# Kernel tuning notes

Measured on AMD Instinct MI355X. Metric: run time of the kernel, lower is better.

## Reference

```python
import jax, jax.numpy as jnp
import numpy as np

N_NODES = 100000
N_EDGES = 1600000
F_IN, F_HID, F_OUT = 512, 128, 64


def add_self_loops(edge_index, num_nodes):
    loop = jnp.arange(num_nodes, dtype=edge_index.dtype)
    loops = jnp.stack([loop, loop])  # [2, N]
    return jnp.concatenate([edge_index, loops], axis=1)


def gcn_conv(x, edge_index_sl, W, b, num_nodes):
    # x: [N, F_in], edge_index_sl: [2, E+N] (self-loops included)
    h = x @ W  # [N, F_out] transform before propagation (PyG GCNConv order)
    src, dst = edge_index_sl[0], edge_index_sl[1]
    ones = jnp.ones(src.shape[0], dtype=h.dtype)
    deg = jax.ops.segment_sum(ones, dst, num_segments=num_nodes)  # in-degree w/ self-loops
    dinv = jnp.where(deg > 0, jax.lax.rsqrt(deg), 0.0)
    norm = dinv[src] * dinv[dst]  # [E+N] symmetric normalization
    msg = h[src] * norm[:, None]  # gather + scale
    out = jax.ops.segment_sum(msg, dst, num_segments=num_nodes)  # scatter-add
    return out + b


def setup_inputs() -> dict:
    key = jax.random.key(0)
    k = jax.random.split(key, 6)
    x = jax.random.normal(k[0], (N_NODES, F_IN), dtype=jnp.float32)
    edge_index = jax.random.randint(k[1], (2, N_EDGES), 0, N_NODES, dtype=jnp.int64)
    W1 = jax.random.normal(k[2], (F_IN, F_HID), dtype=jnp.float32) * (1.0 / np.sqrt(F_IN))
    b1 = jnp.zeros((F_HID,), dtype=jnp.float32)
    W2 = jax.random.normal(k[3], (F_HID, F_OUT), dtype=jnp.float32) * (1.0 / np.sqrt(F_HID))
    b2 = jnp.zeros((F_OUT,), dtype=jnp.float32)
    return {"x": x, "edge_index": edge_index, "W1": W1, "b1": b1, "W2": W2, "b2": b2}


def reference(x, edge_index, W1, b1, W2, b2):
    ei = add_self_loops(edge_index, N_NODES)
    h = jax.nn.relu(gcn_conv(x, ei, W1, b1, N_NODES))
    out = gcn_conv(h, ei, W2, b2, N_NODES)
    return out
```

## Files before the change

### kernel.cpp

```cpp
#include <hip/hip_runtime.h>

#define N_NODES 100000
#define N_EDGES 1600000
#define F_IN 512
#define F_HID 128
#define F_OUT 64

#define BSH 8
#define NBUK 391

typedef unsigned int u32;
typedef __attribute__((ext_vector_type(8))) short bf16x8;
typedef __attribute__((ext_vector_type(4))) float f32x4;

__device__ float g7_bf2f(unsigned short u) {
    return __uint_as_float(((unsigned int)u) << 16);
}

__device__ unsigned short g7_f2bf(float f) {
    unsigned int u = __float_as_uint(f);
    u = u + 0x7fffu + ((u >> 16) & 1u);
    return (unsigned short)(u >> 16);
}

__device__ float2 g7_up(unsigned int u) {
    float2 r;
    r.x = __uint_as_float(u << 16);
    r.y = __uint_as_float(u & 0xffff0000u);
    return r;
}

__device__ static inline void g7_gl2lds16(const void* g, void* l) {
    __builtin_amdgcn_global_load_lds(
        (const __attribute__((address_space(1))) u32*)g,
        (__attribute__((address_space(3))) u32*)l, 16, 0, 0);
}

__global__ void GCN_16716012716713_kernel() {}

__global__ void g7_zero(int* p, int n) {
    int i = blockIdx.x * blockDim.x + threadIdx.x;
    if (i < n) p[i] = 0;
}

__global__ void g7_iprobe(const int* raw, int* iflag) {
    __shared__ int s[256];
    int tid = threadIdx.x;
    int f = 0;
    for (int i = tid; i < 1024; i += 256) {
        if (raw[2 * i + 1] != 0) f = 1;
    }
    s[tid] = f;
    __syncthreads();
    for (int off = 128; off > 0; off >>= 1) {
        if (tid < off) s[tid] |= s[tid + off];
        __syncthreads();
    }
    if (tid == 0) iflag[0] = s[0];
}

__global__ void g7_fprobe(const unsigned int* xw, int* fflag) {
    __shared__ int s[256];
    int tid = threadIdx.x;
    int cnt = 0;
    for (int i = tid; i < 4096; i += 256) {
        unsigned int lo = xw[i] & 0xffffu;
        unsigned int e = (lo >> 7) & 0xffu;
        if (e >= 110u && e <= 140u) cnt = cnt + 1;
    }
    s[tid] = cnt;
    __syncthreads();
    for (int off = 128; off > 0; off >>= 1) {
        if (tid < off) s[tid] += s[tid + off];
        __syncthreads();
    }
    if (tid == 0) fflag[0] = (s[0] > 2048) ? 1 : 0;
}

__global__ void g7_pack(const int* raw, const int* iflag, int* ei, int* deg) {
    int i = blockIdx.x * blockDim.x + threadIdx.x;
    if (i < 2 * N_EDGES) {
        int v;
        if (iflag[0] == 0) {
            v = raw[2 * i];
        } else {
            v = raw[i];
        }
        ei[i] = v;
        if (i >= N_EDGES) atomicAdd(&deg[v], 1);
    }
}

__global__ void g7_cvt(const void* src, const int* fflag, float* dst, int n) {
    int i = blockIdx.x * blockDim.x + threadIdx.x;
    if (i < n) {
        if (fflag[0] == 1) {
            dst[i] = g7_bf2f(((const unsigned short*)src)[i]);
        } else {
            dst[i] = ((const float*)src)[i];
        }
    }
}

__global__ void g7_w1s(const void* W1, const int* fflag,
                       unsigned short* W1Th, unsigned short* W1Tl) {
    int i = blockIdx.x * blockDim.x + threadIdx.x;
    if (i < F_IN * F_HID) {
        int k = i >> 7;
        int n = i & 127;
        float w;
        if (fflag[0] == 1) {
            w = g7_bf2f(((const unsigned short*)W1)[i]);
        } else {
            w = ((const float*)W1)[i];
        }
        unsigned short hi = g7_f2bf(w);
        unsigned short lo = g7_f2bf(w - g7_bf2f(hi));
        W1Th[n * F_IN + k] = hi;
        W1Tl[n * F_IN + k] = lo;
    }
}

__global__ void g7_dinv(const int* deg, float* dinv) {
    int i = blockIdx.x * blockDim.x + threadIdx.x;
    if (i < N_NODES) {
        dinv[i] = rsqrtf((float)deg[i] + 1.0f);
    }
}

__global__ void g7_bsum(const int* deg, int* bsum) {
    __shared__ int s[256];
    int i = blockIdx.x * 256 + threadIdx.x;
    s[threadIdx.x] = (i < N_NODES) ? deg[i] : 0;
    __syncthreads();
    for (int off = 128; off > 0; off >>= 1) {
        if (threadIdx.x < off) s[threadIdx.x] += s[threadIdx.x + off];
        __syncthreads();
    }
    if (threadIdx.x == 0) bsum[blockIdx.x] = s[0];
}

__global__ void g7_bscan(const int* bsum, int* boff, int nblk, int* rowptr) {
    __shared__ int s[512];
    int tid = threadIdx.x;
    int v = (tid < nblk) ? bsum[tid] : 0;
    s[tid] = v;
    __syncthreads();
    for (int off = 1; off < 512; off <<= 1) {
        int t = (tid >= off) ? s[tid - off] : 0;
        __syncthreads();
        s[tid] += t;
        __syncthreads();
    }
    if (tid < nblk) boff[tid] = s[tid] - v;
    if (tid == nblk - 1) rowptr[N_NODES] = s[tid];
}

__global__ void g7_scan(const int* deg, const int* boff, int* rowptr) {
    __shared__ int s[256];
    int i = blockIdx.x * 256 + threadIdx.x;
    int v = (i < N_NODES) ? deg[i] : 0;
    s[threadIdx.x] = v;
    __syncthreads();
    for (int off = 1; off < 256; off <<= 1) {
        int t = (threadIdx.x >= off) ? s[threadIdx.x - off] : 0;
        __syncthreads();
        s[threadIdx.x] += t;
        __syncthreads();
    }
    if (i < N_NODES) {
        rowptr[i] = s[threadIdx.x] - v + boff[blockIdx.x];
    }
}

__global__ void g7_binit(const int* rowptr, int* bcur) {
    int b = blockIdx.x * blockDim.x + threadIdx.x;
    if (b < NBUK) bcur[b] = rowptr[b << BSH];
}

#define P1_EPT 32
#define P1_TILE (256 * P1_EPT)
__global__ void g7_part1(const int* ei, int* bcur, uint2* part) {
    __shared__ int cnt[NBUK + 1];
    __shared__ int base[NBUK + 1];
    int tid = threadIdx.x;
    long long t0 = (long long)blockIdx.x * P1_TILE;
    for (int i = tid; i < NBUK; i += 256) cnt[i] = 0;
    __syncthreads();
#pragma unroll 4
    for (int r = 0; r < P1_EPT; ++r) {
        long long e = t0 + r * 256 + tid;
        if (e < N_EDGES) {
            int d = ei[N_EDGES + e];
            atomicAdd(&cnt[d >> BSH], 1);
        }
    }
    __syncthreads();
    for (int i = tid; i < NBUK; i += 256) {
        int c = cnt[i];
        base[i] = (c > 0) ? atomicAdd(&bcur[i], c) : 0;
        cnt[i] = 0;
    }
    __syncthreads();
#pragma unroll 4
    for (int r = 0; r < P1_EPT; ++r) {
        long long e = t0 + r * 256 + tid;
        if (e < N_EDGES) {
            int s = ei[e];
            int d = ei[N_EDGES + e];
            int bk = d >> BSH;
            int off = atomicAdd(&cnt[bk], 1);
            uint2 p; p.x = (u32)s; p.y = (u32)d;
            part[(long long)base[bk] + off] = p;
        }
    }
}

__global__ void g7_part2(const int* rowptr, const uint2* part, int* csr) {
    __shared__ int lcur[256];
    int b = blockIdx.x;
    int tid = threadIdx.x;
    int n0 = b << BSH;
    int n1 = n0 + 256; if (n1 > N_NODES) n1 = N_NODES;
    if (tid < 256) {
        int node = n0 + tid;
        lcur[tid] = (node < N_NODES) ? rowptr[node] : 0;
    }
    __syncthreads();
    int beg = rowptr[n0];
    int end = rowptr[n1];
    for (int j = beg + tid; j < end; j += 512) {
        uint2 p = part[j];
        int pos = atomicAdd(&lcur[p.y - n0], 1);
        csr[pos] = (int)p.x;
    }
}

__global__ __launch_bounds__(256, 2) void g7_gemm1s(const void* x, const int* fflag,
        const unsigned short* W1Th, const unsigned short* W1Tl, unsigned short* h1b) {
    __shared__ uint4 smv[4096];
    char* smc = (char*)smv;
    int tid = threadIdx.x;
    int m0 = blockIdx.x * 128;
    int w = tid >> 6;
    int lane = tid & 63;
    int wr = w >> 1, wc = w & 1;
    int la = lane & 15;
    int lk = lane >> 4;
    int isbf = fflag[0];
    int ar = tid >> 1;
    int ah = tid & 1;

    f32x4 acc[4][4];
#pragma unroll
    for (int i = 0; i < 4; ++i)
#pragma unroll
        for (int j = 0; j < 4; ++j) acc[i][j] = (f32x4){0.f, 0.f, 0.f, 0.f};

    uint4 rA[4];

    auto loadA = [&](int k0) {
        int m = m0 + ar;
        if (m >= N_NODES) m = N_NODES - 1;
        if (isbf) {
            const char* s = (const char*)x + ((long long)m * F_IN + k0 + ah * 16) * 2;
            rA[0] = *(const uint4*)s;
            rA[1] = *(const uint4*)(s + 16);
        } else {
            const char* s = (const char*)x + ((long long)m * F_IN + k0 + ah * 16) * 4;
            rA[0] = *(const uint4*)s;
            rA[1] = *(const uint4*)(s + 16);
            rA[2] = *(const uint4*)(s + 32);
            rA[3] = *(const uint4*)(s + 48);
        }
    };

    auto writeA = [&](char* As) {
        float f[16];
        if (isbf) {
            const unsigned short* p = (const unsigned short*)rA;
#pragma unroll
            for (int j = 0; j < 16; ++j) f[j] = g7_bf2f(p[j]);
        } else {
            const float* p = (const float*)rA;
#pragma unroll
            for (int j = 0; j < 16; ++j) f[j] = p[j];
        }
        unsigned int hw[8], lw[8];
#pragma unroll
        for (int j = 0; j < 8; ++j) {
            unsigned short h0 = g7_f2bf(f[2 * j]);
            unsigned short h1v = g7_f2bf(f[2 * j + 1]);
            unsigned short l0 = g7_f2bf(f[2 * j] - g7_bf2f(h0));
            unsigned short l1 = g7_f2bf(f[2 * j + 1] - g7_bf2f(h1v));
            hw[j] = (unsigned int)h0 | ((unsigned int)h1v << 16);
            lw[j] = (unsigned int)l0 | ((unsigned int)l1 << 16);
        }
        int swz = (ar & 7) << 4;
        char* dst = As + ar * 128;
        *(uint4*)(dst + ((ah * 32 + 0) ^ swz))      = make_uint4(hw[0], hw[1], hw[2], hw[3]);
        *(uint4*)(dst + ((ah * 32 + 16) ^ swz))     = make_uint4(hw[4], hw[5], hw[6], hw[7]);
        *(uint4*)(dst + ((64 + ah * 32 + 0) ^ swz)) = make_uint4(lw[0], lw[1], lw[2], lw[3]);
        *(uint4*)(dst + ((64 + ah * 32 + 16) ^ swz))= make_uint4(lw[4], lw[5], lw[6], lw[7]);
    };

    auto stageB = [&](char* Bs, int k0) {
#pragma unroll
        for (int p = 0; p < 4; ++p) {
            int nr = w * 32 + p * 8 + (lane >> 3);
            int cp = ((lane & 7) * 16) ^ (((lane >> 3) & 7) << 4);
            const char* src = (cp < 64)
                ? (const char*)W1Th + (long long)nr * 1024 + k0 * 2 + cp
                : (const char*)W1Tl + (long long)nr * 1024 + k0 * 2 + (cp - 64);
            g7_gl2lds16(src, Bs + (w * 32 + p * 8) * 128);
        }
    };

    auto compute = [&](const char* As, const char* Bs) {
        bf16x8 a_hi[4], a_lo[4], b_hi[4], b_lo[4];
#pragma unroll
        for (int i = 0; i < 4; ++i) {
            int r = wr * 64 + i * 16 + la;
            int swz = (r & 7) << 4;
            const char* ab = As + r * 128;
            a_hi[i] = *(const bf16x8*)(ab + ((lk * 16) ^ swz));
            a_lo[i] = *(const bf16x8*)(ab + ((64 + lk * 16) ^ swz));
            int n = wc * 64 + i * 16 + la;
            int swzb = (n & 7) << 4;
            const char* bb = Bs + n * 128;
            b_hi[i] = *(const bf16x8*)(bb + ((lk * 16) ^ swzb));
            b_lo[i] = *(const bf16x8*)(bb + ((64 + lk * 16) ^ swzb));
        }
#pragma unroll
        for (int i = 0; i < 4; ++i)
#pragma unroll
            for (int j = 0; j < 4; ++j) {
                acc[i][j] = __builtin_amdgcn_mfma_f32_16x16x32_bf16(
                    a_hi[i], b_hi[j], acc[i][j], 0, 0, 0);
                acc[i][j] = __builtin_amdgcn_mfma_f32_16x16x32_bf16(
                    a_lo[i], b_hi[j], acc[i][j], 0, 0, 0);
                acc[i][j] = __builtin_amdgcn_mfma_f32_16x16x32_bf16(
                    a_hi[i], b_lo[j], acc[i][j], 0, 0, 0);
            }
    };

    loadA(0);
    stageB(smc + 16384, 0);
    writeA(smc);
    __syncthreads();

    for (int kt = 0; kt < 16; ++kt) {
        char* bc = smc + (kt & 1) * 32768;
        char* bn = smc + ((kt & 1) ^ 1) * 32768;
        if (kt < 15) {
            loadA((kt + 1) * 32);
            stageB(bn + 16384, (kt + 1) * 32);
        }
        compute(bc, bc + 16384);
        if (kt < 15) writeA(bn);
        __syncthreads();
    }

#pragma unroll
    for (int i = 0; i < 4; ++i) {
#pragma unroll
        for (int j = 0; j < 4; ++j) {
            int n = wc * 64 + j * 16 + la;
#pragma unroll
            for (int q = 0; q < 4; ++q) {
                int m = m0 + wr * 64 + i * 16 + lk * 4 + q;
                if (m < N_NODES) {
                    h1b[(long long)m * F_HID + n] = g7_f2bf(acc[i][j][q]);
                }
            }
        }
    }
}

__global__ void g7_agg1(const int* rowptr, const int* csr, const float* dinv,
                        const unsigned short* h1b, const float* b1, float* r1) {
    int node = blockIdx.x * 4 + (threadIdx.x >> 6);
    int lane = threadIdx.x & 63;
    int e = lane >> 5;
    int fl = lane & 31;
    if (node >= N_NODES) return;
    int beg = rowptr[node];
    int end = rowptr[node + 1];
    const uint2* hv = (const uint2*)h1b;
    float a0 = 0.f, a1 = 0.f, a2 = 0.f, a3 = 0.f;
    int j = beg + e;
    for (; j + 2 < end; j += 4) {
        int s0 = csr[j];
        int s1 = csr[j + 2];
        float w0 = dinv[s0];
        float w1 = dinv[s1];
        uint2 v0 = hv[(long long)s0 * 32 + fl];
        uint2 v1 = hv[(long long)s1 * 32 + fl];
        float2 p0 = g7_up(v0.x), q0 = g7_up(v0.y);
        float2 p1 = g7_up(v1.x), q1 = g7_up(v1.y);
        a0 += p0.x * w0 + p1.x * w1;
        a1 += p0.y * w0 + p1.y * w1;
        a2 += q0.x * w0 + q1.x * w1;
        a3 += q0.y * w0 + q1.y * w1;
    }
    if (j < end) {
        int s0 = csr[j];
        float w0 = dinv[s0];
        uint2 v0 = hv[(long long)s0 * 32 + fl];
        float2 p0 = g7_up(v0.x), q0 = g7_up(v0.y);
        a0 += p0.x * w0;
        a1 += p0.y * w0;
        a2 += q0.x * w0;
        a3 += q0.y * w0;
    }
    float di = dinv[node];
    if (e == 0) {
        uint2 vd = hv[(long long)node * 32 + fl];
        float2 pd = g7_up(vd.x), qd = g7_up(vd.y);
        a0 += pd.x * di;
        a1 += pd.y * di;
        a2 += qd.x * di;
        a3 += qd.y * di;
    }
    a0 += __shfl_xor(a0, 32);
    a1 += __shfl_xor(a1, 32);
    a2 += __shfl_xor(a2, 32);
    a3 += __shfl_xor(a3, 32);
    if (e == 0) {
        float4 bb = *(const float4*)(b1 + 4 * fl);
        float r0 = a0 * di + bb.x;
        float r1v = a1 * di + bb.y;
        float r2 = a2 * di + bb.z;
        float r3 = a3 * di + bb.w;
        if (r0 < 0.f) r0 = 0.f;
        if (r1v < 0.f) r1v = 0.f;
        if (r2 < 0.f) r2 = 0.f;
        if (r3 < 0.f) r3 = 0.f;
        float4 o;
        o.x = r0; o.y = r1v; o.z = r2; o.w = r3;
        *(float4*)(r1 + (long long)node * F_HID + 4 * fl) = o;
    }
}

__global__ void g7_gemm2(const float* r1, const float* W2, unsigned short* h2b) {
    __shared__ float Rs[32][68];
    __shared__ float Ws[32][64];
    int tid = threadIdx.x;
    int m0 = blockIdx.x * 64;
    int tx = tid & 15;
    int ty = tid >> 4;
    float acc[4][4];
#pragma unroll
    for (int i = 0; i < 4; ++i) {
#pragma unroll
        for (int j = 0; j < 4; ++j) acc[i][j] = 0.0f;
    }

    for (int k0 = 0; k0 < F_HID; k0 += 32) {
#pragma unroll
        for (int r = 0; r < 8; ++r) {
            int i = r * 256 + tid;
            int kk = i & 31;
            int mm = i >> 5;
            int m = m0 + mm;
            float v = 0.0f;
            if (m < N_NODES) {
                v = r1[(long long)m * F_HID + k0 + kk];
            }
            Rs[kk][mm] = v;
        }
#pragma unroll
        for (int r = 0; r < 8; ++r) {
            int i = r * 256 + tid;
            int wk = i >> 6;
            int wn = i & 63;
            Ws[wk][wn] = W2[(k0 + wk) * F_OUT + wn];
        }
        __syncthreads();
#pragma unroll
        for (int k = 0; k < 32; ++k) {
            float a[4];
            float b[4];
#pragma unroll
            for (int i = 0; i < 4; ++i) a[i] = Rs[k][ty * 4 + i];
#pragma unroll
            for (int j = 0; j < 4; ++j) b[j] = Ws[k][tx * 4 + j];
#pragma unroll
            for (int i = 0; i < 4; ++i) {
#pragma unroll
                for (int j = 0; j < 4; ++j) acc[i][j] += a[i] * b[j];
            }
        }
        __syncthreads();
    }
#pragma unroll
    for (int i = 0; i < 4; ++i) {
        int m = m0 + ty * 4 + i;
        if (m < N_NODES) {
            unsigned int w0 = (unsigned int)g7_f2bf(acc[i][0])
                            | ((unsigned int)g7_f2bf(acc[i][1]) << 16);
            unsigned int w1 = (unsigned int)g7_f2bf(acc[i][2])
                            | ((unsigned int)g7_f2bf(acc[i][3]) << 16);
            uint2 o; o.x = w0; o.y = w1;
            *(uint2*)(h2b + (long long)m * F_OUT + tx * 4) = o;
        }
    }
}

__global__ void g7_agg2(const int* rowptr, const int* csr, const float* dinv,
                        const unsigned short* h2b, const float* b2, const int* fflag,
                        void* out) {
    int node = blockIdx.x * 4 + (threadIdx.x >> 6);
    int lane = threadIdx.x & 63;
    int e = lane >> 5;
    int fl = lane & 31;
    if (node >= N_NODES) return;
    int beg = rowptr[node];
    int end = rowptr[node + 1];
    const u32* hv = (const u32*)h2b;
    float a0 = 0.f, a1 = 0.f;
    int j = beg + e;
    for (; j + 2 < end; j += 4) {
        int s0 = csr[j];
        int s1 = csr[j + 2];
        float w0 = dinv[s0];
        float w1 = dinv[s1];
        u32 v0 = hv[(long long)s0 * 32 + fl];
        u32 v1 = hv[(long long)s1 * 32 + fl];
        float2 p0 = g7_up(v0);
        float2 p1 = g7_up(v1);
        a0 += p0.x * w0 + p1.x * w1;
        a1 += p0.y * w0 + p1.y * w1;
    }
    if (j < end) {
        int s0 = csr[j];
        float w0 = dinv[s0];
        u32 v0 = hv[(long long)s0 * 32 + fl];
        float2 p0 = g7_up(v0);
        a0 += p0.x * w0;
        a1 += p0.y * w0;
    }
    float di = dinv[node];
    if (e == 0) {
        u32 vd = hv[(long long)node * 32 + fl];
        float2 pd = g7_up(vd);
        a0 += pd.x * di;
        a1 += pd.y * di;
    }
    a0 += __shfl_xor(a0, 32);
    a1 += __shfl_xor(a1, 32);
    if (e == 0) {
        float v0 = a0 * di + b2[2 * fl];
        float v1 = a1 * di + b2[2 * fl + 1];
        long long oi = (long long)node * F_OUT + 2 * fl;
        if (fflag[0] == 1) {
            u32 o = (u32)g7_f2bf(v0) | ((u32)g7_f2bf(v1) << 16);
            *(u32*)((unsigned short*)out + oi) = o;
        } else {
            float2 o; o.x = v0; o.y = v1;
            *(float2*)((float*)out + oi) = o;
        }
    }
}

extern "C" void kernel_launch(void* const* d_in, const int* in_sizes, int n_in,
                              void* d_out, int out_size, void* d_ws, size_t ws_size,
                              hipStream_t stream) {
    const void* x     = d_in[0];
    const int* ei_raw = (const int*)d_in[1];
    const void* W1    = d_in[2];
    const void* b1    = d_in[3];
    const void* W2    = d_in[4];
    const void* b2    = d_in[5];

    const int NBLK = (N_NODES + 255) / 256;

    char* ws = (char*)d_ws;
    int*   deg    = (int*)(ws + 0);
    int*   iflag  = (int*)(ws + 409600);
    int*   fflag  = (int*)(ws + 409616);
    int*   bsum   = (int*)(ws + 409632);
    int*   boff   = (int*)(ws + 412800);
    int*   bcur   = (int*)(ws + 450560);
    float* dinv   = (float*)(ws + 524288);
    unsigned short* W1Th = (unsigned short*)(ws + 1048576);
    unsigned short* W1Tl = (unsigned short*)(ws + 1179648);
    float* b1f    = (float*)(ws + 1310720);
    float* W2f    = (float*)(ws + 1311232);
    float* b2f    = (float*)(ws + 1344000);
    int*   ei     = (int*)(ws + 2097152);
    int*   rowptr = (int*)(ws + 14897152);
    int*   csr    = (int*)(ws + 16777216);
    unsigned short* h1b = (unsigned short*)(ws + 23177216);
    uint2* part   = (uint2*)(ws + 50331648);
    float* r1     = (float*)(ws + 74377216);
    unsigned short* h2b = (unsigned short*)(ws + 125577216);

    g7_zero<<<(N_NODES + 255) / 256, 256, 0, stream>>>(deg, N_NODES);

    g7_iprobe<<<1, 256, 0, stream>>>(ei_raw, iflag);
    g7_fprobe<<<1, 256, 0, stream>>>((const unsigned int*)x, fflag);

    g7_pack<<<(2 * N_EDGES + 255) / 256, 256, 0, stream>>>(ei_raw, iflag, ei, deg);

    g7_cvt<<<1, 128, 0, stream>>>(b1, fflag, b1f, F_HID);
    g7_cvt<<<(F_HID * F_OUT + 255) / 256, 256, 0, stream>>>(W2, fflag, W2f, F_HID * F_OUT);
    g7_cvt<<<1, 64, 0, stream>>>(b2, fflag, b2f, F_OUT);
    g7_w1s<<<(F_IN * F_HID + 255) / 256, 256, 0, stream>>>(W1, fflag, W1Th, W1Tl);

    g7_dinv<<<(N_NODES + 255) / 256, 256, 0, stream>>>(deg, dinv);

    g7_bsum<<<NBLK, 256, 0, stream>>>(deg, bsum);
    g7_bscan<<<1, 512, 0, stream>>>(bsum, boff, NBLK, rowptr);
    g7_scan<<<NBLK, 256, 0, stream>>>(deg, boff, rowptr);

    g7_binit<<<(NBUK + 255) / 256, 256, 0, stream>>>(rowptr, bcur);
    g7_part1<<<(N_EDGES + P1_TILE - 1) / P1_TILE, 256, 0, stream>>>(ei, bcur, part);
    g7_part2<<<NBUK, 512, 0, stream>>>(rowptr, part, csr);

    g7_gemm1s<<<(N_NODES + 127) / 128, 256, 0, stream>>>(x, fflag, W1Th, W1Tl, h1b);

    g7_agg1<<<N_NODES / 4, 256, 0, stream>>>(rowptr, csr, dinv, h1b, b1f, r1);

    g7_gemm2<<<(N_NODES + 63) / 64, 256, 0, stream>>>(r1, W2f, h2b);

    g7_agg2<<<N_NODES / 4, 256, 0, stream>>>(rowptr, csr, dinv, h2b, b2f, fflag, d_out);
}
```

Measured before the change: 648.5 us.

## Single-buffer LDS in gemm1 and raise occupancy to four blocks per CU

The first GEMM kernel goes from a double-buffered 64KB LDS layout to a single 32KB A/B buffer. Prefetching now happens through two register buffers for A, and launch bounds rise from 2 to 4 blocks per CU. The goal is to hide memory latency through higher occupancy instead of LDS double buffering. In exchange, each k-step now needs two barriers, the B global-to-LDS copy is no longer overlapped with compute, and the tighter register budget may cause spills.

```diff
diff --git a/kernel.cpp b/kernel.cpp
--- a/kernel.cpp
+++ b/kernel.cpp
@@ -236,10 +236,11 @@
     }
 }
 
-__global__ __launch_bounds__(256, 2) void g7_gemm1s(const void* x, const int* fflag,
+__global__ __launch_bounds__(256, 4) void g7_gemm1s(const void* x, const int* fflag,
         const unsigned short* W1Th, const unsigned short* W1Tl, unsigned short* h1b) {
-    __shared__ uint4 smv[4096];
-    char* smc = (char*)smv;
+    __shared__ uint4 smv[2048];
+    char* As = (char*)smv;
+    char* Bs = As + 16384;
     int tid = threadIdx.x;
     int m0 = blockIdx.x * 128;
     int w = tid >> 6;
@@ -257,9 +258,9 @@
 #pragma unroll
         for (int j = 0; j < 4; ++j) acc[i][j] = (f32x4){0.f, 0.f, 0.f, 0.f};
 
-    uint4 rA[4];
-
-    auto loadA = [&](int k0) {
+    uint4 rA0[4], rA1[4];
+
+    auto loadA = [&](uint4* rA, int k0) {
         int m = m0 + ar;
         if (m >= N_NODES) m = N_NODES - 1;
         if (isbf) {
@@ -275,7 +276,7 @@
         }
     };
 
-    auto writeA = [&](char* As) {
+    auto writeA = [&](const uint4* rA) {
         float f[16];
         if (isbf) {
             const unsigned short* p = (const unsigned short*)rA;
@@ -304,7 +305,7 @@
         *(uint4*)(dst + ((64 + ah * 32 + 16) ^ swz))= make_uint4(lw[4], lw[5], lw[6], lw[7]);
     };
 
-    auto stageB = [&](char* Bs, int k0) {
+    auto stageB = [&](int k0) {
 #pragma unroll
         for (int p = 0; p < 4; ++p) {
             int nr = w * 32 + p * 8 + (lane >> 3);
@@ -316,7 +317,7 @@
         }
     };
 
-    auto compute = [&](const char* As, const char* Bs) {
+    auto compute = [&]() {
         bf16x8 a_hi[4], a_lo[4], b_hi[4], b_lo[4];
 #pragma unroll
         for (int i = 0; i < 4; ++i) {
@@ -344,20 +345,20 @@
             }
     };
 
-    loadA(0);
-    stageB(smc + 16384, 0);
-    writeA(smc);
-    __syncthreads();
-
-    for (int kt = 0; kt < 16; ++kt) {
-        char* bc = smc + (kt & 1) * 32768;
-        char* bn = smc + ((kt & 1) ^ 1) * 32768;
-        if (kt < 15) {
-            loadA((kt + 1) * 32);
-            stageB(bn + 16384, (kt + 1) * 32);
-        }
-        compute(bc, bc + 16384);
-        if (kt < 15) writeA(bn);
+    loadA(rA0, 0);
+#pragma unroll
+    for (int kt = 0; kt < 16; kt += 2) {
+        writeA(rA0);
+        stageB(kt * 32);
+        __syncthreads();
+        loadA(rA1, (kt + 1) * 32);
+        compute();
+        __syncthreads();
+        writeA(rA1);
+        stageB((kt + 1) * 32);
+        __syncthreads();
+        if (kt + 2 < 16) loadA(rA0, (kt + 2) * 32);
+        compute();
         __syncthreads();
     }
 
```

Measured after the change: 732.7 us. 13.0% more time.

## Use 512-thread GEMM1 blocks with smaller per-wave tiles and fuse weight-prep kernels

Applied to the files above, without the earlier changes.

The first GEMM now runs 8 waves per 128x128 tile instead of 4, so each wave owns a 64x32 output sub-tile with half the accumulators. Each thread loads and splits half as much A data. The launch bound moves from (256,2) to (512,4) to raise occupancy and latency hiding. Separately, the three small conversion kernels and the W1 split kernel are merged into a single prep launch to cut launch overhead. With more waves per tile, A fragments are reloaded from shared memory by more waves, which adds LDS traffic.

```diff
diff --git a/kernel.cpp b/kernel.cpp
--- a/kernel.cpp
+++ b/kernel.cpp
@@ -91,25 +91,16 @@
     }
 }
 
-__global__ void g7_cvt(const void* src, const int* fflag, float* dst, int n) {
+__global__ void g7_prep(const void* W1, const void* W2, const void* b1, const void* b2,
+                        const int* fflag, unsigned short* W1Th, unsigned short* W1Tl,
+                        float* W2f, float* b1f, float* b2f) {
     int i = blockIdx.x * blockDim.x + threadIdx.x;
-    if (i < n) {
-        if (fflag[0] == 1) {
-            dst[i] = g7_bf2f(((const unsigned short*)src)[i]);
-        } else {
-            dst[i] = ((const float*)src)[i];
-        }
-    }
-}
-
-__global__ void g7_w1s(const void* W1, const int* fflag,
-                       unsigned short* W1Th, unsigned short* W1Tl) {
-    int i = blockIdx.x * blockDim.x + threadIdx.x;
+    int isbf = fflag[0];
     if (i < F_IN * F_HID) {
         int k = i >> 7;
         int n = i & 127;
         float w;
-        if (fflag[0] == 1) {
+        if (isbf == 1) {
             w = g7_bf2f(((const unsigned short*)W1)[i]);
         } else {
             w = ((const float*)W1)[i];
@@ -118,6 +109,18 @@
         unsigned short lo = g7_f2bf(w - g7_bf2f(hi));
         W1Th[n * F_IN + k] = hi;
         W1Tl[n * F_IN + k] = lo;
+    } else if (i < F_IN * F_HID + F_HID * F_OUT) {
+        int j = i - F_IN * F_HID;
+        W2f[j] = (isbf == 1) ? g7_bf2f(((const unsigned short*)W2)[j])
+                             : ((const float*)W2)[j];
+    } else if (i < F_IN * F_HID + F_HID * F_OUT + F_HID) {
+        int j = i - F_IN * F_HID - F_HID * F_OUT;
+        b1f[j] = (isbf == 1) ? g7_bf2f(((const unsigned short*)b1)[j])
+                             : ((const float*)b1)[j];
+    } else if (i < F_IN * F_HID + F_HID * F_OUT + F_HID + F_OUT) {
+        int j = i - F_IN * F_HID - F_HID * F_OUT - F_HID;
+        b2f[j] = (isbf == 1) ? g7_bf2f(((const unsigned short*)b2)[j])
+                             : ((const float*)b2)[j];
     }
 }
 
@@ -236,7 +239,7 @@
     }
 }
 
-__global__ __launch_bounds__(256, 2) void g7_gemm1s(const void* x, const int* fflag,
+__global__ __launch_bounds__(512, 4) void g7_gemm1s(const void* x, const int* fflag,
         const unsigned short* W1Th, const unsigned short* W1Tl, unsigned short* h1b) {
     __shared__ uint4 smv[4096];
     char* smc = (char*)smv;
@@ -244,51 +247,48 @@
     int m0 = blockIdx.x * 128;
     int w = tid >> 6;
     int lane = tid & 63;
-    int wr = w >> 1, wc = w & 1;
+    int wr = w >> 2, wc = w & 3;
     int la = lane & 15;
     int lk = lane >> 4;
     int isbf = fflag[0];
-    int ar = tid >> 1;
-    int ah = tid & 1;
-
-    f32x4 acc[4][4];
+    int ar = tid >> 2;
+    int ah = tid & 3;
+
+    f32x4 acc[4][2];
 #pragma unroll
     for (int i = 0; i < 4; ++i)
 #pragma unroll
-        for (int j = 0; j < 4; ++j) acc[i][j] = (f32x4){0.f, 0.f, 0.f, 0.f};
-
-    uint4 rA[4];
+        for (int j = 0; j < 2; ++j) acc[i][j] = (f32x4){0.f, 0.f, 0.f, 0.f};
+
+    uint4 rA[2];
 
     auto loadA = [&](int k0) {
         int m = m0 + ar;
         if (m >= N_NODES) m = N_NODES - 1;
         if (isbf) {
-            const char* s = (const char*)x + ((long long)m * F_IN + k0 + ah * 16) * 2;
+            const char* s = (const char*)x + ((long long)m * F_IN + k0 + ah * 8) * 2;
+            rA[0] = *(const uint4*)s;
+        } else {
+            const char* s = (const char*)x + ((long long)m * F_IN + k0 + ah * 8) * 4;
             rA[0] = *(const uint4*)s;
             rA[1] = *(const uint4*)(s + 16);
-        } else {
-            const char* s = (const char*)x + ((long long)m * F_IN + k0 + ah * 16) * 4;
-            rA[0] = *(const uint4*)s;
-            rA[1] = *(const uint4*)(s + 16);
-            rA[2] = *(const uint4*)(s + 32);
-            rA[3] = *(const uint4*)(s + 48);
         }
     };
 
     auto writeA = [&](char* As) {
-        float f[16];
+        float f[8];
         if (isbf) {
-            const unsigned short* p = (const unsigned short*)rA;
-#pragma unroll
-            for (int j = 0; j < 16; ++j) f[j] = g7_bf2f(p[j]);
+            const unsigned short* p = (const unsigned short*)&rA[0];
+#pragma unroll
+            for (int j = 0; j < 8; ++j) f[j] = g7_bf2f(p[j]);
         } else {
             const float* p = (const float*)rA;
 #pragma unroll
-            for (int j = 0; j < 16; ++j) f[j] = p[j];
-        }
-        unsigned int hw[8], lw[8];
-#pragma unroll
-        for (int j = 0; j < 8; ++j) {
+            for (int j = 0; j < 8; ++j) f[j] = p[j];
+        }
+        unsigned int hw[4], lw[4];
+#pragma unroll
+        for (int j = 0; j < 4; ++j) {
             unsigned short h0 = g7_f2bf(f[2 * j]);
             unsigned short h1v = g7_f2bf(f[2 * j + 1]);
             unsigned short l0 = g7_f2bf(f[2 * j] - g7_bf2f(h0));
@@ -298,50 +298,49 @@
         }
         int swz = (ar & 7) << 4;
         char* dst = As + ar * 128;
-        *(uint4*)(dst + ((ah * 32 + 0) ^ swz))      = make_uint4(hw[0], hw[1], hw[2], hw[3]);
-        *(uint4*)(dst + ((ah * 32 + 16) ^ swz))     = make_uint4(hw[4], hw[5], hw[6], hw[7]);
-        *(uint4*)(dst + ((64 + ah * 32 + 0) ^ swz)) = make_uint4(lw[0], lw[1], lw[2], lw[3]);
-        *(uint4*)(dst + ((64 + ah * 32 + 16) ^ swz))= make_uint4(lw[4], lw[5], lw[6], lw[7]);
+        *(uint4*)(dst + ((ah * 16) ^ swz))      = make_uint4(hw[0], hw[1], hw[2], hw[3]);
+        *(uint4*)(dst + ((64 + ah * 16) ^ swz)) = make_uint4(lw[0], lw[1], lw[2], lw[3]);
     };
 
     auto stageB = [&](char* Bs, int k0) {
 #pragma unroll
-        for (int p = 0; p < 4; ++p) {
-            int nr = w * 32 + p * 8 + (lane >> 3);
+        for (int p = 0; p < 2; ++p) {
+            int nr = w * 16 + p * 8 + (lane >> 3);
             int cp = ((lane & 7) * 16) ^ (((lane >> 3) & 7) << 4);
             const char* src = (cp < 64)
                 ? (const char*)W1Th + (long long)nr * 1024 + k0 * 2 + cp
                 : (const char*)W1Tl + (long long)nr * 1024 + k0 * 2 + (cp - 64);
-            g7_gl2lds16(src, Bs + (w * 32 + p * 8) * 128);
+            g7_gl2lds16(src, Bs + (w * 16 + p * 8) * 128);
         }
     };
 
     auto compute = [&](const char* As, const char* Bs) {
-        bf16x8 a_hi[4], a_lo[4], b_hi[4], b_lo[4];
+        bf16x8 bh[2], bl[2];
+#pragma unroll
+        for (int j = 0; j < 2; ++j) {
+            int n = wc * 32 + j * 16 + la;
+            int swzb = (n & 7) << 4;
+            const char* bb = Bs + n * 128;
+            bh[j] = *(const bf16x8*)(bb + ((lk * 16) ^ swzb));
+            bl[j] = *(const bf16x8*)(bb + ((64 + lk * 16) ^ swzb));
+        }
 #pragma unroll
         for (int i = 0; i < 4; ++i) {
             int r = wr * 64 + i * 16 + la;
             int swz = (r & 7) << 4;
             const char* ab = As + r * 128;
-            a_hi[i] = *(const bf16x8*)(ab + ((lk * 16) ^ swz));
-            a_lo[i] = *(const bf16x8*)(ab + ((64 + lk * 16) ^ swz));
-            int n = wc * 64 + i * 16 + la;
-            int swzb = (n & 7) << 4;
-            const char* bb = Bs + n * 128;
-            b_hi[i] = *(const bf16x8*)(bb + ((lk * 16) ^ swzb));
-            b_lo[i] = *(const bf16x8*)(bb + ((64 + lk * 16) ^ swzb));
-        }
-#pragma unroll
-        for (int i = 0; i < 4; ++i)
-#pragma unroll
-            for (int j = 0; j < 4; ++j) {
+            bf16x8 ah_ = *(const bf16x8*)(ab + ((lk * 16) ^ swz));
+            bf16x8 al_ = *(const bf16x8*)(ab + ((64 + lk * 16) ^ swz));
+#pragma unroll
+            for (int j = 0; j < 2; ++j) {
                 acc[i][j] = __builtin_amdgcn_mfma_f32_16x16x32_bf16(
-                    a_hi[i], b_hi[j], acc[i][j], 0, 0, 0);
+                    ah_, bh[j], acc[i][j], 0, 0, 0);
                 acc[i][j] = __builtin_amdgcn_mfma_f32_16x16x32_bf16(
-                    a_lo[i], b_hi[j], acc[i][j], 0, 0, 0);
+                    al_, bh[j], acc[i][j], 0, 0, 0);
                 acc[i][j] = __builtin_amdgcn_mfma_f32_16x16x32_bf16(
-                    a_hi[i], b_lo[j], acc[i][j], 0, 0, 0);
+                    ah_, bl[j], acc[i][j], 0, 0, 0);
             }
+        }
     };
 
     loadA(0);
@@ -364,8 +363,8 @@
 #pragma unroll
     for (int i = 0; i < 4; ++i) {
 #pragma unroll
-        for (int j = 0; j < 4; ++j) {
-            int n = wc * 64 + j * 16 + la;
+        for (int j = 0; j < 2; ++j) {
+            int n = wc * 32 + j * 16 + la;
 #pragma unroll
             for (int q = 0; q < 4; ++q) {
                 int m = m0 + wr * 64 + i * 16 + lk * 4 + q;
@@ -603,10 +602,9 @@
 
     g7_pack<<<(2 * N_EDGES + 255) / 256, 256, 0, stream>>>(ei_raw, iflag, ei, deg);
 
-    g7_cvt<<<1, 128, 0, stream>>>(b1, fflag, b1f, F_HID);
-    g7_cvt<<<(F_HID * F_OUT + 255) / 256, 256, 0, stream>>>(W2, fflag, W2f, F_HID * F_OUT);
-    g7_cvt<<<1, 64, 0, stream>>>(b2, fflag, b2f, F_OUT);
-    g7_w1s<<<(F_IN * F_HID + 255) / 256, 256, 0, stream>>>(W1, fflag, W1Th, W1Tl);
+    const int PREP_N = F_IN * F_HID + F_HID * F_OUT + F_HID + F_OUT;
+    g7_prep<<<(PREP_N + 255) / 256, 256, 0, stream>>>(W1, W2, b1, b2, fflag,
+                                                      W1Th, W1Tl, W2f, b1f, b2f);
 
     g7_dinv<<<(N_NODES + 255) / 256, 256, 0, stream>>>(deg, dinv);
 
@@ -618,7 +616,7 @@
     g7_part1<<<(N_EDGES + P1_TILE - 1) / P1_TILE, 256, 0, stream>>>(ei, bcur, part);
     g7_part2<<<NBUK, 512, 0, stream>>>(rowptr, part, csr);
 
-    g7_gemm1s<<<(N_NODES + 127) / 128, 256, 0, stream>>>(x, fflag, W1Th, W1Tl, h1b);
+    g7_gemm1s<<<(N_NODES + 127) / 128, 512, 0, stream>>>(x, fflag, W1Th, W1Tl, h1b);
 
     g7_agg1<<<N_NODES / 4, 256, 0, stream>>>(rowptr, csr, dinv, h1b, b1f, r1);
 
```

Measured after the change: 631.0 us. 2.7% less time.
